# Performance work log

Measured on AMD Instinct MI355X. Metric: run time of the kernel, lower is better.

## Reference

```python
import jax, jax.numpy as jnp
import numpy as np

SIZE = 7
SIGMA = 1.5
CHANNELS = 1
K1 = 0.01
K2 = 0.03
NP_ = SIZE * SIZE
COV_NORM = NP_ / (NP_ - 1)


def gaussian_window(size=SIZE, sigma=SIGMA, channels=CHANNELS):
    x = jnp.arange(size, dtype=jnp.float32) - size // 2
    g = jnp.exp(-x ** 2 / (2.0 * sigma ** 2))[None, :]  # [1, size]
    w = (g.T @ g)  # [size, size]
    w = w / jnp.sum(w)
    return jnp.broadcast_to(w[None, None], (channels, 1, size, size))  # [C,1,k,k]


def _blur(x, w, pad):
    # depthwise conv2d, groups == channels
    return jax.lax.conv_general_dilated(
        x, w, window_strides=(1, 1), padding=[(pad, pad), (pad, pad)],
        dimension_numbers=('NCHW', 'OIHW', 'NCHW'),
        feature_group_count=x.shape[1])


def setup_inputs() -> dict:
    key = jax.random.key(0)
    k1, k2 = jax.random.split(key)
    B, C, H, W = 64, CHANNELS, 512, 512
    X = jax.random.uniform(k1, (B, C, H, W), dtype=jnp.float32)
    Y = jax.random.uniform(k2, (B, C, H, W), dtype=jnp.float32)
    window = gaussian_window()
    return {"X": X, "Y": Y, "window": window}


def reference(X, Y, window):
    B = Y.shape[0]
    Yf = Y.reshape(B, -1)
    data_range = (jnp.max(Yf, axis=1) - jnp.min(Yf, axis=1)).reshape(B, 1, 1, 1)
    C1 = (K1 * data_range) ** 2
    C2 = (K2 * data_range) ** 2
    pad = SIZE // 2
    mux = _blur(X, window, pad)
    muy = _blur(Y, window, pad)
    mux_sq = mux * mux
    muy_sq = muy * muy
    muxy = mux * muy
    sigmax_sq = (_blur(X * X, window, pad) - mux_sq) * COV_NORM
    sigmay_sq = (_blur(Y * Y, window, pad) - muy_sq) * COV_NORM
    sigmaxy = (_blur(X * Y, window, pad) - muxy) * COV_NORM
    ssim_map = (2 * muxy + C1) * (2 * sigmaxy + C2) / ((mux_sq + muy_sq + C1) * (sigmax_sq + sigmay_sq + C2))
    return 1.0 - jnp.mean(ssim_map)
```

## Files before the change

### kernel.cpp

```cpp
#include <hip/hip_runtime.h>
#include <math.h>


__device__ __forceinline__ unsigned fkey(float f) {
    unsigned u = __float_as_uint(f);
    return (u & 0x80000000u) ? ~u : (u | 0x80000000u);
}
__device__ __forceinline__ float funkey(unsigned k) {
    return __uint_as_float((k & 0x80000000u) ? (k & 0x7FFFFFFFu) : ~k);
}

__global__ void init_ws(const float* __restrict__ w, float* __restrict__ u7,
                        unsigned* __restrict__ mink, unsigned* __restrict__ maxk,
                        double* __restrict__ sum) {
    int t = threadIdx.x;
    if (t == 0) *sum = 0.0;
    if (t < 64) { mink[t] = 0xFFFFFFFFu; maxk[t] = 0u; }
    if (t < 7) {
        float s = 0.f;
        for (int j = 0; j < 7; ++j) s += w[t * 7 + j];
        u7[t] = s;
    }
}

__global__ __launch_bounds__(256) void minmax_kernel(const float4* __restrict__ Y,
                                                     unsigned* __restrict__ mink,
                                                     unsigned* __restrict__ maxk) {
    int b = blockIdx.x >> 4, ch = blockIdx.x & 15;
    const float4* p = Y + (size_t)b * 65536 + (size_t)ch * 4096 + threadIdx.x;
    float lmin = INFINITY, lmax = -INFINITY;
#pragma unroll
    for (int i = 0; i < 16; ++i) {
        float4 v = p[(size_t)i * 256];
        lmin = fminf(lmin, fminf(fminf(v.x, v.y), fminf(v.z, v.w)));
        lmax = fmaxf(lmax, fmaxf(fmaxf(v.x, v.y), fmaxf(v.z, v.w)));
    }
#pragma unroll
    for (int off = 32; off; off >>= 1) {
        lmin = fminf(lmin, __shfl_down(lmin, off));
        lmax = fmaxf(lmax, __shfl_down(lmax, off));
    }
    if ((threadIdx.x & 63) == 0) {
        atomicMin(&mink[b], fkey(lmin));
        atomicMax(&maxk[b], fkey(lmax));
    }
}

__global__ __launch_bounds__(256, 4) void ssim_kernel(const float* __restrict__ X,
                                                      const float* __restrict__ Yg,
                                                      const float* __restrict__ u7,
                                                      const unsigned* __restrict__ mink,
                                                      const unsigned* __restrict__ maxk,
                                                      double* __restrict__ sum) {
    __shared__ float2 s[2][264];
    __shared__ float warpsum[4];

    const int blk = blockIdx.x;
    const int b   = blk >> 5;
    const int sub = blk & 31;
    const int cs  = sub & 1;
    const int rs  = sub >> 1;
    const int c0  = cs << 8;
    const int r0  = rs << 5;
    const int t   = threadIdx.x;

    float u[7];
#pragma unroll
    for (int i = 0; i < 7; ++i) u[i] = u7[i];

    const float dr = funkey(maxk[b]) - funkey(mink[b]);
    float C1 = 0.01f * dr; C1 *= C1;
    float C2 = 0.03f * dr; C2 *= C2;
    const float cn = 49.f / 48.f;

    const float* __restrict__ Xb = X  + ((size_t)b << 18);
    const float* __restrict__ Yb = Yg + ((size_t)b << 18);

    const int  c    = c0 + t;
    const bool hasE = (t < 6);
    const int  eL   = (t < 3) ? t : (t + 256);
    const int  ecol = c0 + eL - 3;
    const bool eok  = (ecol >= 0) && (ecol < 512);
    const int  ec   = min(max(ecol, 0), 511);

    float pxr[2], pyr[2], pxe[2], pye[2];
    float phx[7], phy[7], phxx[7], phyy[7], phxy[7];
    float ssacc = 0.f;

#define LOADROW(P, JJ) do {                                                   \
    int r_ = r0 - 3 + (JJ);                                                   \
    if (r_ >= 0 && r_ < 512) {                                                \
        const float* xp_ = Xb + ((size_t)r_ << 9);                            \
        const float* yp_ = Yb + ((size_t)r_ << 9);                            \
        pxr[(P)] = xp_[c]; pyr[(P)] = yp_[c];                                 \
        if (hasE) { pxe[(P)] = eok ? xp_[ec] : 0.f;                           \
                    pye[(P)] = eok ? yp_[ec] : 0.f; }                         \
    } else {                                                                  \
        pxr[(P)] = 0.f; pyr[(P)] = 0.f; pxe[(P)] = 0.f; pye[(P)] = 0.f;       \
    }                                                                         \
} while (0)

#define WRITEROW(P) do {                                                      \
    s[(P)][t + 3] = make_float2(pxr[(P)], pyr[(P)]);                          \
    if (hasE) s[(P)][eL] = make_float2(pxe[(P)], pye[(P)]);                   \
} while (0)

#define HBLUR(BUF, SLOT) do {                                                 \
    float hx_ = 0.f, hy_ = 0.f, hxx_ = 0.f, hyy_ = 0.f, hxy_ = 0.f;           \
    _Pragma("unroll")                                                         \
    for (int k_ = 0; k_ < 7; ++k_) {                                          \
        float2 v_ = s[(BUF)][t + k_];                                         \
        float wx_ = u[k_] * v_.x, wy_ = u[k_] * v_.y;                         \
        hx_ += wx_; hy_ += wy_;                                               \
        hxx_ = fmaf(wx_, v_.x, hxx_);                                         \
        hxy_ = fmaf(wx_, v_.y, hxy_);                                         \
        hyy_ = fmaf(wy_, v_.y, hyy_);                                         \
    }                                                                         \
    phx[(SLOT)] = hx_; phy[(SLOT)] = hy_;                                     \
    phxx[(SLOT)] = hxx_; phyy[(SLOT)] = hyy_; phxy[(SLOT)] = hxy_;            \
} while (0)

#define VS(a, J) fmaf(u[6], a[(J) % 7], fmaf(u[5], a[((J)+6) % 7],            \
               fmaf(u[4], a[((J)+5) % 7], fmaf(u[3], a[((J)+4) % 7],          \
               fmaf(u[2], a[((J)+3) % 7], fmaf(u[1], a[((J)+2) % 7],          \
               u[0] * a[((J)+1) % 7]))))))

#define EMIT(J) do {                                                          \
    float mux = VS(phx, (J)), muy = VS(phy, (J));                             \
    float mxx = VS(phxx, (J)), myy = VS(phyy, (J)), mxy = VS(phxy, (J));      \
    float mux2 = mux * mux, muy2 = muy * muy, muxy = mux * muy;               \
    float sxx = (mxx - mux2) * cn;                                            \
    float syy = (myy - muy2) * cn;                                            \
    float sxy = (mxy - muxy) * cn;                                            \
    float num = (2.f * muxy + C1) * (2.f * sxy + C2);                         \
    float den = (mux2 + muy2 + C1) * (sxx + syy + C2);                        \
    ssacc = fmaf(num, __builtin_amdgcn_rcpf(den), ssacc);                     \
} while (0)

#define PSTEP(J) do {                                                         \
    HBLUR((J) & 1, (J) % 7);                                                  \
    WRITEROW(((J) + 1) & 1);                                                  \
    LOADROW(((J) + 1) & 1, (J) + 3);                                          \
    __syncthreads();                                                          \
} while (0)

#define MSTEP(J) do {                                                         \
    HBLUR((J) & 1, (J) % 7);                                                  \
    EMIT(J);                                                                  \
    WRITEROW(((J) + 1) & 1);                                                  \
    LOADROW(((J) + 1) & 1, jb + (J) + 3);                                     \
    __syncthreads();                                                          \
} while (0)

#define MSTEP_NL(J) do {                                  \
    HBLUR((J) & 1, (J) % 7);                                                  \
    EMIT(J);                                                                  \
    WRITEROW(((J) + 1) & 1);                                                  \
    __syncthreads();                                                          \
} while (0)

#define MSTEP_END(J) do {                 \
    HBLUR((J) & 1, (J) % 7);                                                  \
    EMIT(J);                                                                  \
} while (0)

    LOADROW(0, 0);
    LOADROW(1, 1);
    WRITEROW(0);
    LOADROW(0, 2);
    __syncthreads();

    PSTEP(0); PSTEP(1); PSTEP(2); PSTEP(3); PSTEP(4); PSTEP(5);

    for (int g = 0; g < 2; ++g) {
        const int jb = 14 * g;
        MSTEP(6);  MSTEP(7);  MSTEP(8);  MSTEP(9);  MSTEP(10); MSTEP(11); MSTEP(12);
        MSTEP(13); MSTEP(14); MSTEP(15); MSTEP(16); MSTEP(17); MSTEP(18); MSTEP(19);
    }

    {
        const int jb = 28;
        MSTEP(6);
        MSTEP_NL(7);
        MSTEP_NL(8);
        MSTEP_END(9);
    }

#undef LOADROW
#undef WRITEROW
#undef HBLUR
#undef VS
#undef EMIT
#undef PSTEP
#undef MSTEP
#undef MSTEP_NL
#undef MSTEP_END

#pragma unroll
    for (int off = 32; off; off >>= 1) ssacc += __shfl_down(ssacc, off);
    if ((t & 63) == 0) warpsum[t >> 6] = ssacc;
    __syncthreads();
    if (t == 0) {
        double sm = (double)warpsum[0] + (double)warpsum[1] +
                    (double)warpsum[2] + (double)warpsum[3];
        atomicAdd(sum, sm);
    }
}

__global__ void finalize_kernel(const double* __restrict__ sum, float* __restrict__ out) {
    out[0] = (float)(1.0 - (*sum) / (64.0 * 512.0 * 512.0));
}

extern "C" void kernel_launch(void* const* d_in, const int* in_sizes, int n_in,
                              void* d_out, int out_size, void* d_ws, size_t ws_size,
                              hipStream_t stream) {
    const float* X = (const float*)d_in[0];
    const float* Y = (const float*)d_in[1];
    const float* W = (const float*)d_in[2];

    char* ws = (char*)d_ws;
    double* sum = (double*)(ws + 0);
    unsigned* mink = (unsigned*)(ws + 16);
    unsigned* maxk = (unsigned*)(ws + 16 + 256);
    float* u7 = (float*)(ws + 16 + 512);

    init_ws<<<1, 64, 0, stream>>>(W, u7, mink, maxk, sum);
    minmax_kernel<<<1024, 256, 0, stream>>>((const float4*)Y, mink, maxk);
    ssim_kernel<<<2048, 256, 0, stream>>>(X, Y, u7, mink, maxk, sum);
    finalize_kernel<<<1, 1, 0, stream>>>(sum, (float*)d_out);
}
```

Measured before the change: 93.63 us.

## Process two columns per thread with full-row blocks and float2 loads

Each thread now computes two adjacent output columns and each block covers the full 512-column row, so the column-halo exchange and the edge-thread loads go away. Global loads become float2 and shared-memory rows are stored as float4 with zero padding, which lets eight loaded values feed two horizontal blurs. The grid is halved and the occupancy hint is removed from the launch bounds. In exchange, each thread holds twice as many partial sums in registers, which may lower occupancy.

```diff
diff --git a/kernel.cpp b/kernel.cpp
--- a/kernel.cpp
+++ b/kernel.cpp
@@ -46,21 +46,18 @@
     }
 }
 
-__global__ __launch_bounds__(256, 4) void ssim_kernel(const float* __restrict__ X,
-                                                      const float* __restrict__ Yg,
-                                                      const float* __restrict__ u7,
-                                                      const unsigned* __restrict__ mink,
-                                                      const unsigned* __restrict__ maxk,
-                                                      double* __restrict__ sum) {
-    __shared__ float2 s[2][264];
+__global__ __launch_bounds__(256) void ssim_kernel(const float* __restrict__ X,
+                                                   const float* __restrict__ Yg,
+                                                   const float* __restrict__ u7,
+                                                   const unsigned* __restrict__ mink,
+                                                   const unsigned* __restrict__ maxk,
+                                                   double* __restrict__ sum) {
+    __shared__ float4 s4[2][260];
     __shared__ float warpsum[4];
 
     const int blk = blockIdx.x;
-    const int b   = blk >> 5;
-    const int sub = blk & 31;
-    const int cs  = sub & 1;
-    const int rs  = sub >> 1;
-    const int c0  = cs << 8;
+    const int b   = blk >> 4;
+    const int rs  = blk & 15;
     const int r0  = rs << 5;
     const int t   = threadIdx.x;
 
@@ -76,48 +73,62 @@
     const float* __restrict__ Xb = X  + ((size_t)b << 18);
     const float* __restrict__ Yb = Yg + ((size_t)b << 18);
 
-    const int  c    = c0 + t;
-    const bool hasE = (t < 6);
-    const int  eL   = (t < 3) ? t : (t + 256);
-    const int  ecol = c0 + eL - 3;
-    const bool eok  = (ecol >= 0) && (ecol < 512);
-    const int  ec   = min(max(ecol, 0), 511);
-
-    float pxr[2], pyr[2], pxe[2], pye[2];
-    float phx[7], phy[7], phxx[7], phyy[7], phxy[7];
+    if (t < 2) {
+        float4 z = make_float4(0.f, 0.f, 0.f, 0.f);
+        s4[0][t] = z; s4[1][t] = z;
+        s4[0][258 + t] = z; s4[1][258 + t] = z;
+    }
+
+    float2 fx[2], fy[2];
+    float phx0[7], phy0[7], phxx0[7], phyy0[7], phxy0[7];
+    float phx1[7], phy1[7], phxx1[7], phyy1[7], phxy1[7];
     float ssacc = 0.f;
 
 #define LOADROW(P, JJ) do {                                                   \
     int r_ = r0 - 3 + (JJ);                                                   \
-    if (r_ >= 0 && r_ < 512) {                                                \
-        const float* xp_ = Xb + ((size_t)r_ << 9);                            \
-        const float* yp_ = Yb + ((size_t)r_ << 9);                            \
-        pxr[(P)] = xp_[c]; pyr[(P)] = yp_[c];                                 \
-        if (hasE) { pxe[(P)] = eok ? xp_[ec] : 0.f;                           \
-                    pye[(P)] = eok ? yp_[ec] : 0.f; }                         \
+    if (r_ >= 0 && r_ < 512) {                      \
+        const float2* xp_ = (const float2*)(Xb + ((size_t)r_ << 9)) + t;      \
+        const float2* yp_ = (const float2*)(Yb + ((size_t)r_ << 9)) + t;      \
+        fx[(P)] = *xp_; fy[(P)] = *yp_;                                       \
     } else {                                                                  \
-        pxr[(P)] = 0.f; pyr[(P)] = 0.f; pxe[(P)] = 0.f; pye[(P)] = 0.f;       \
+        fx[(P)] = make_float2(0.f, 0.f); fy[(P)] = make_float2(0.f, 0.f);     \
     }                                                                         \
 } while (0)
 
 #define WRITEROW(P) do {                                                      \
-    s[(P)][t + 3] = make_float2(pxr[(P)], pyr[(P)]);                          \
-    if (hasE) s[(P)][eL] = make_float2(pxe[(P)], pye[(P)]);                   \
+    s4[(P)][t + 2] = make_float4(fx[(P)].x, fy[(P)].x, fx[(P)].y, fy[(P)].y); \
 } while (0)
 
 #define HBLUR(BUF, SLOT) do {                                                 \
-    float hx_ = 0.f, hy_ = 0.f, hxx_ = 0.f, hyy_ = 0.f, hxy_ = 0.f;           \
+    const float2* sb_ = (const float2*)s4[(BUF)];                             \
+    float2 v_[8];                                                             \
     _Pragma("unroll")                                                         \
-    for (int k_ = 0; k_ < 7; ++k_) {                                          \
-        float2 v_ = s[(BUF)][t + k_];                                         \
-        float wx_ = u[k_] * v_.x, wy_ = u[k_] * v_.y;                         \
-        hx_ += wx_; hy_ += wy_;                                               \
-        hxx_ = fmaf(wx_, v_.x, hxx_);                                         \
-        hxy_ = fmaf(wx_, v_.y, hxy_);                                         \
-        hyy_ = fmaf(wy_, v_.y, hyy_);                                         \
-    }                                                                         \
-    phx[(SLOT)] = hx_; phy[(SLOT)] = hy_;                                     \
-    phxx[(SLOT)] = hxx_; phyy[(SLOT)] = hyy_; phxy[(SLOT)] = hxy_;            \
+    for (int k_ = 0; k_ < 8; ++k_) v_[k_] = sb_[(t << 1) + 1 + k_];           \
+    float hx0_=0.f, hy0_=0.f, hxx0_=0.f, hyy0_=0.f, hxy0_=0.f;                \
+    float hx1_=0.f, hy1_=0.f, hxx1_=0.f, hyy1_=0.f, hxy1_=0.f;                \
+    _Pragma("unroll")                                                         \
+    for (int k_ = 0; k_ < 8; ++k_) {                                          \
+        float xv_ = v_[k_].x, yv_ = v_[k_].y;                                 \
+        float xx_ = xv_ * xv_, yy_ = yv_ * yv_, xy_ = xv_ * yv_;              \
+        if (k_ < 7) {                                                         \
+            hx0_  = fmaf(u[k_], xv_, hx0_);                                   \
+            hy0_  = fmaf(u[k_], yv_, hy0_);                                   \
+            hxx0_ = fmaf(u[k_], xx_, hxx0_);                                  \
+            hyy0_ = fmaf(u[k_], yy_, hyy0_);                                  \
+            hxy0_ = fmaf(u[k_], xy_, hxy0_);                                  \
+        }                                                                     \
+        if (k_ > 0) {                                                         \
+            hx1_  = fmaf(u[k_ - 1], xv_, hx1_);                               \
+            hy1_  = fmaf(u[k_ - 1], yv_, hy1_);                               \
+            hxx1_ = fmaf(u[k_ - 1], xx_, hxx1_);                              \
+            hyy1_ = fmaf(u[k_ - 1], yy_, hyy1_);                              \
+            hxy1_ = fmaf(u[k_ - 1], xy_, hxy1_);                              \
+        }                                                                     \
+    }                                                                         \
+    phx0[(SLOT)] = hx0_; phy0[(SLOT)] = hy0_; phxx0[(SLOT)] = hxx0_;          \
+    phyy0[(SLOT)] = hyy0_; phxy0[(SLOT)] = hxy0_;                             \
+    phx1[(SLOT)] = hx1_; phy1[(SLOT)] = hy1_; phxx1[(SLOT)] = hxx1_;          \
+    phyy1[(SLOT)] = hyy1_; phxy1[(SLOT)] = hxy1_;                             \
 } while (0)
 
 #define VS(a, J) fmaf(u[6], a[(J) % 7], fmaf(u[5], a[((J)+6) % 7],            \
@@ -125,16 +136,27 @@
                fmaf(u[2], a[((J)+3) % 7], fmaf(u[1], a[((J)+2) % 7],          \
                u[0] * a[((J)+1) % 7]))))))
 
-#define EMIT(J) do {                                                          \
-    float mux = VS(phx, (J)), muy = VS(phy, (J));                             \
-    float mxx = VS(phxx, (J)), myy = VS(phyy, (J)), mxy = VS(phxy, (J));      \
-    float mux2 = mux * mux, muy2 = muy * muy, muxy = mux * muy;               \
-    float sxx = (mxx - mux2) * cn;                                            \
-    float syy = (myy - muy2) * cn;                                            \
-    float sxy = (mxy - muxy) * cn;                                            \
+#define SSIM1(mux, muy, mxx, myy, mxy) do {                                   \
+    float mux2 = (mux) * (mux), muy2 = (muy) * (muy), muxy = (mux) * (muy);   \
+    float sxx = ((mxx) - mux2) * cn;                                          \
+    float syy = ((myy) - muy2) * cn;                                          \
+    float sxy = ((mxy) - muxy) * cn;                                          \
     float num = (2.f * muxy + C1) * (2.f * sxy + C2);                         \
     float den = (mux2 + muy2 + C1) * (sxx + syy + C2);                        \
     ssacc = fmaf(num, __builtin_amdgcn_rcpf(den), ssacc);                     \
+} while (0)
+
+#define EMIT(J) do {                                                          \
+    {                                                                         \
+        float mux = VS(phx0, (J)), muy = VS(phy0, (J));                       \
+        float mxx = VS(phxx0, (J)), myy = VS(phyy0, (J)), mxy = VS(phxy0, (J));\
+        SSIM1(mux, muy, mxx, myy, mxy);                                       \
+    }                                                                         \
+    {                                                                         \
+        float mux = VS(phx1, (J)), muy = VS(phy1, (J));                       \
+        float mxx = VS(phxx1, (J)), myy = VS(phyy1, (J)), mxy = VS(phxy1, (J));\
+        SSIM1(mux, muy, mxx, myy, mxy);                                       \
+    }                                                                         \
 } while (0)
 
 #define PSTEP(J) do {                                                         \
@@ -152,14 +174,14 @@
     __syncthreads();                                                          \
 } while (0)
 
-#define MSTEP_NL(J) do {                                  \
+#define MSTEP_NL(J) do {                                                      \
     HBLUR((J) & 1, (J) % 7);                                                  \
     EMIT(J);                                                                  \
     WRITEROW(((J) + 1) & 1);                                                  \
     __syncthreads();                                                          \
 } while (0)
 
-#define MSTEP_END(J) do {                 \
+#define MSTEP_END(J) do {                                                     \
     HBLUR((J) & 1, (J) % 7);                                                  \
     EMIT(J);                                                                  \
 } while (0)
@@ -190,6 +212,7 @@
 #undef WRITEROW
 #undef HBLUR
 #undef VS
+#undef SSIM1
 #undef EMIT
 #undef PSTEP
 #undef MSTEP
@@ -226,6 +249,6 @@
 
     init_ws<<<1, 64, 0, stream>>>(W, u7, mink, maxk, sum);
     minmax_kernel<<<1024, 256, 0, stream>>>((const float4*)Y, mink, maxk);
-    ssim_kernel<<<2048, 256, 0, stream>>>(X, Y, u7, mink, maxk, sum);
+    ssim_kernel<<<1024, 256, 0, stream>>>(X, Y, u7, mink, maxk, sum);
     finalize_kernel<<<1, 1, 0, stream>>>(sum, (float*)d_out);
 }
```

Result: slower. 130.6 us (+39.5%).

## Merge xx and yy blur channels and double the row tile per block

Applied to the files above, without the earlier changes.

The SSIM formula only needs the sum of the x² and y² blurs, so the kernel precomputes x²+y² and x·y per pixel when writing to shared memory. The horizontal and vertical blurs then run over four channels instead of five, using float4 LDS reads. Each block also covers 64 rows instead of 32, which halves the grid and cuts the relative cost of the 6-row halo reloads. The trade-off is fewer blocks to spread across CUs, and a small change in rounding from combining the sums first.

```diff
diff --git a/kernel.cpp b/kernel.cpp
--- a/kernel.cpp
+++ b/kernel.cpp
@@ -52,16 +52,16 @@
                                                       const unsigned* __restrict__ mink,
                                                       const unsigned* __restrict__ maxk,
                                                       double* __restrict__ sum) {
-    __shared__ float2 s[2][264];
+    __shared__ float4 s4[2][262];
     __shared__ float warpsum[4];
 
     const int blk = blockIdx.x;
-    const int b   = blk >> 5;
-    const int sub = blk & 31;
+    const int b   = blk >> 4;
+    const int sub = blk & 15;
     const int cs  = sub & 1;
     const int rs  = sub >> 1;
     const int c0  = cs << 8;
-    const int r0  = rs << 5;
+    const int r0  = rs << 6;
     const int t   = threadIdx.x;
 
     float u[7];
@@ -71,7 +71,8 @@
     const float dr = funkey(maxk[b]) - funkey(mink[b]);
     float C1 = 0.01f * dr; C1 *= C1;
     float C2 = 0.03f * dr; C2 *= C2;
-    const float cn = 49.f / 48.f;
+    const float cn  = 49.f / 48.f;
+    const float cn2 = 2.f * cn;
 
     const float* __restrict__ Xb = X  + ((size_t)b << 18);
     const float* __restrict__ Yb = Yg + ((size_t)b << 18);
@@ -83,41 +84,46 @@
     const bool eok  = (ecol >= 0) && (ecol < 512);
     const int  ec   = min(max(ecol, 0), 511);
 
-    float pxr[2], pyr[2], pxe[2], pye[2];
-    float phx[7], phy[7], phxx[7], phyy[7], phxy[7];
+    float fx[2], fy[2], ex[2], ey[2];
+    float phx[7], phy[7], phq[7], phxy[7];
     float ssacc = 0.f;
 
 #define LOADROW(P, JJ) do {                                                   \
     int r_ = r0 - 3 + (JJ);                                                   \
-    if (r_ >= 0 && r_ < 512) {                                                \
+    if (r_ >= 0 && r_ < 512) {                      \
         const float* xp_ = Xb + ((size_t)r_ << 9);                            \
         const float* yp_ = Yb + ((size_t)r_ << 9);                            \
-        pxr[(P)] = xp_[c]; pyr[(P)] = yp_[c];                                 \
-        if (hasE) { pxe[(P)] = eok ? xp_[ec] : 0.f;                           \
-                    pye[(P)] = eok ? yp_[ec] : 0.f; }                         \
+        fx[(P)] = xp_[c]; fy[(P)] = yp_[c];                                   \
+        if (hasE) { ex[(P)] = eok ? xp_[ec] : 0.f;                            \
+                    ey[(P)] = eok ? yp_[ec] : 0.f; }                          \
     } else {                                                                  \
-        pxr[(P)] = 0.f; pyr[(P)] = 0.f; pxe[(P)] = 0.f; pye[(P)] = 0.f;       \
+        fx[(P)] = 0.f; fy[(P)] = 0.f; ex[(P)] = 0.f; ey[(P)] = 0.f;           \
     }                                                                         \
 } while (0)
 
 #define WRITEROW(P) do {                                                      \
-    s[(P)][t + 3] = make_float2(pxr[(P)], pyr[(P)]);                          \
-    if (hasE) s[(P)][eL] = make_float2(pxe[(P)], pye[(P)]);                   \
+    float q_  = fmaf(fx[(P)], fx[(P)], fy[(P)] * fy[(P)]);                    \
+    float xy_ = fx[(P)] * fy[(P)];                                            \
+    s4[(P)][t + 3] = make_float4(fx[(P)], fy[(P)], q_, xy_);                  \
+    if (hasE) {                                                               \
+        float qe_  = fmaf(ex[(P)], ex[(P)], ey[(P)] * ey[(P)]);               \
+        float xye_ = ex[(P)] * ey[(P)];                                       \
+        s4[(P)][eL] = make_float4(ex[(P)], ey[(P)], qe_, xye_);               \
+    }                                                                         \
 } while (0)
 
 #define HBLUR(BUF, SLOT) do {                                                 \
-    float hx_ = 0.f, hy_ = 0.f, hxx_ = 0.f, hyy_ = 0.f, hxy_ = 0.f;           \
+    float hx_ = 0.f, hy_ = 0.f, hq_ = 0.f, hxy_ = 0.f;                        \
     _Pragma("unroll")                                                         \
     for (int k_ = 0; k_ < 7; ++k_) {                                          \
-        float2 v_ = s[(BUF)][t + k_];                                         \
-        float wx_ = u[k_] * v_.x, wy_ = u[k_] * v_.y;                         \
-        hx_ += wx_; hy_ += wy_;                                               \
-        hxx_ = fmaf(wx_, v_.x, hxx_);                                         \
-        hxy_ = fmaf(wx_, v_.y, hxy_);                                         \
-        hyy_ = fmaf(wy_, v_.y, hyy_);                                         \
+        float4 v_ = s4[(BUF)][t + k_];                                        \
+        hx_  = fmaf(u[k_], v_.x, hx_);                                        \
+        hy_  = fmaf(u[k_], v_.y, hy_);                                        \
+        hq_  = fmaf(u[k_], v_.z, hq_);                                        \
+        hxy_ = fmaf(u[k_], v_.w, hxy_);                                       \
     }                                                                         \
     phx[(SLOT)] = hx_; phy[(SLOT)] = hy_;                                     \
-    phxx[(SLOT)] = hxx_; phyy[(SLOT)] = hyy_; phxy[(SLOT)] = hxy_;            \
+    phq[(SLOT)] = hq_; phxy[(SLOT)] = hxy_;                                   \
 } while (0)
 
 #define VS(a, J) fmaf(u[6], a[(J) % 7], fmaf(u[5], a[((J)+6) % 7],            \
@@ -127,14 +133,14 @@
 
 #define EMIT(J) do {                                                          \
     float mux = VS(phx, (J)), muy = VS(phy, (J));                             \
-    float mxx = VS(phxx, (J)), myy = VS(phyy, (J)), mxy = VS(phxy, (J));      \
+    float mq  = VS(phq, (J)), mxy = VS(phxy, (J));                            \
     float mux2 = mux * mux, muy2 = muy * muy, muxy = mux * muy;               \
-    float sxx = (mxx - mux2) * cn;                                            \
-    float syy = (myy - muy2) * cn;                                            \
-    float sxy = (mxy - muxy) * cn;                                            \
-    float num = (2.f * muxy + C1) * (2.f * sxy + C2);                         \
-    float den = (mux2 + muy2 + C1) * (sxx + syy + C2);                        \
-    ssacc = fmaf(num, __builtin_amdgcn_rcpf(den), ssacc);                     \
+    float m2 = mux2 + muy2;                                                   \
+    float A_ = fmaf(muxy, 2.f, C1);                   \
+    float B_ = fmaf(mxy - muxy, cn2, C2);             \
+    float D_ = m2 + C1;                                                       \
+    float E_ = fmaf(mq - m2, cn, C2);                 \
+    ssacc = fmaf(A_ * B_, __builtin_amdgcn_rcpf(D_ * E_), ssacc);             \
 } while (0)
 
 #define PSTEP(J) do {                                                         \
@@ -152,14 +158,14 @@
     __syncthreads();                                                          \
 } while (0)
 
-#define MSTEP_NL(J) do {                                  \
+#define MSTEP_NL(J) do {                                                      \
     HBLUR((J) & 1, (J) % 7);                                                  \
     EMIT(J);                                                                  \
     WRITEROW(((J) + 1) & 1);                                                  \
     __syncthreads();                                                          \
 } while (0)
 
-#define MSTEP_END(J) do {                 \
+#define MSTEP_END(J) do {                                                     \
     HBLUR((J) & 1, (J) % 7);                                                  \
     EMIT(J);                                                                  \
 } while (0)
@@ -172,18 +178,22 @@
 
     PSTEP(0); PSTEP(1); PSTEP(2); PSTEP(3); PSTEP(4); PSTEP(5);
 
-    for (int g = 0; g < 2; ++g) {
+    for (int g = 0; g < 4; ++g) {
         const int jb = 14 * g;
         MSTEP(6);  MSTEP(7);  MSTEP(8);  MSTEP(9);  MSTEP(10); MSTEP(11); MSTEP(12);
         MSTEP(13); MSTEP(14); MSTEP(15); MSTEP(16); MSTEP(17); MSTEP(18); MSTEP(19);
     }
 
     {
-        const int jb = 28;
+        const int jb = 56;
         MSTEP(6);
-        MSTEP_NL(7);
-        MSTEP_NL(8);
-        MSTEP_END(9);
+        MSTEP(7);
+        MSTEP(8);
+        MSTEP(9);
+        MSTEP(10);
+        MSTEP_NL(11);
+        MSTEP_NL(12);
+        MSTEP_END(13);
     }
 
 #undef LOADROW
@@ -226,6 +236,6 @@
 
     init_ws<<<1, 64, 0, stream>>>(W, u7, mink, maxk, sum);
     minmax_kernel<<<1024, 256, 0, stream>>>((const float4*)Y, mink, maxk);
-    ssim_kernel<<<2048, 256, 0, stream>>>(X, Y, u7, mink, maxk, sum);
+    ssim_kernel<<<1024, 256, 0, stream>>>(X, Y, u7, mink, maxk, sum);
     finalize_kernel<<<1, 1, 0, stream>>>(sum, (float*)d_out);
 }
```

Result: slower. 108.2 us (+15.6%).

## Give each wavefront a private LDS strip and drop block-wide barriers

Applied to the files above, without the earlier changes.

Splits the 256-column block tile into four independent 64-column strips, one per wavefront. Each strip has its own double-buffered LDS rows with a 6-column halo. The per-row __syncthreads calls are removed and replaced by compiler memory barriers, relying on lockstep execution inside a 64-lane wavefront. This removes block-wide synchronisation stalls on every row step. In exchange, each wave loads its own halo columns, so redundant global loads and LDS writes increase, and correctness now depends on wavefront-synchronous LDS ordering.

```diff
diff --git a/kernel.cpp b/kernel.cpp
--- a/kernel.cpp
+++ b/kernel.cpp
@@ -52,17 +52,21 @@
                                                       const unsigned* __restrict__ mink,
                                                       const unsigned* __restrict__ maxk,
                                                       double* __restrict__ sum) {
-    __shared__ float2 s[2][264];
+    __shared__ float2 s[4][2][72];
     __shared__ float warpsum[4];
 
-    const int blk = blockIdx.x;
-    const int b   = blk >> 5;
-    const int sub = blk & 31;
-    const int cs  = sub & 1;
-    const int rs  = sub >> 1;
-    const int c0  = cs << 8;
-    const int r0  = rs << 5;
-    const int t   = threadIdx.x;
+    const int blk  = blockIdx.x;
+    const int b    = blk >> 5;
+    const int sub  = blk & 31;
+    const int cs   = sub & 1;
+    const int rs   = sub >> 1;
+    const int t    = threadIdx.x;
+    const int wv   = t >> 6;
+    const int lane = t & 63;
+    const int c0   = (cs << 8) + (wv << 6);
+    const int r0   = rs << 5;
+
+    float2 (* __restrict__ sw)[72] = s[wv];
 
     float u[7];
 #pragma unroll
@@ -76,40 +80,44 @@
     const float* __restrict__ Xb = X  + ((size_t)b << 18);
     const float* __restrict__ Yb = Yg + ((size_t)b << 18);
 
-    const int  c    = c0 + t;
-    const bool hasE = (t < 6);
-    const int  eL   = (t < 3) ? t : (t + 256);
+    const int  c    = c0 + lane;
+    const bool hasE = (lane < 6);
+    const int  eL   = (lane < 3) ? lane : (lane + 64);
     const int  ecol = c0 + eL - 3;
     const bool eok  = (ecol >= 0) && (ecol < 512);
     const int  ec   = min(max(ecol, 0), 511);
 
-    float pxr[2], pyr[2], pxe[2], pye[2];
+    float fx[2], fy[2], ex[2], ey[2];
     float phx[7], phy[7], phxx[7], phyy[7], phxy[7];
     float ssacc = 0.f;
 
+#define CBAR asm volatile("" ::: "memory")
+
 #define LOADROW(P, JJ) do {                                                   \
     int r_ = r0 - 3 + (JJ);                                                   \
-    if (r_ >= 0 && r_ < 512) {                                                \
+    if (r_ >= 0 && r_ < 512) {                      \
         const float* xp_ = Xb + ((size_t)r_ << 9);                            \
         const float* yp_ = Yb + ((size_t)r_ << 9);                            \
-        pxr[(P)] = xp_[c]; pyr[(P)] = yp_[c];                                 \
-        if (hasE) { pxe[(P)] = eok ? xp_[ec] : 0.f;                           \
-                    pye[(P)] = eok ? yp_[ec] : 0.f; }                         \
+        fx[(P)] = xp_[c]; fy[(P)] = yp_[c];                                   \
+        if (hasE) { ex[(P)] = eok ? xp_[ec] : 0.f;                            \
+                    ey[(P)] = eok ? yp_[ec] : 0.f; }                          \
     } else {                                                                  \
-        pxr[(P)] = 0.f; pyr[(P)] = 0.f; pxe[(P)] = 0.f; pye[(P)] = 0.f;       \
+        fx[(P)] = 0.f; fy[(P)] = 0.f; ex[(P)] = 0.f; ey[(P)] = 0.f;           \
     }                                                                         \
 } while (0)
 
 #define WRITEROW(P) do {                                                      \
-    s[(P)][t + 3] = make_float2(pxr[(P)], pyr[(P)]);                          \
-    if (hasE) s[(P)][eL] = make_float2(pxe[(P)], pye[(P)]);                   \
+    CBAR;                                                                     \
+    sw[(P)][lane + 3] = make_float2(fx[(P)], fy[(P)]);                        \
+    if (hasE) sw[(P)][eL] = make_float2(ex[(P)], ey[(P)]);                    \
+    CBAR;                                                                     \
 } while (0)
 
 #define HBLUR(BUF, SLOT) do {                                                 \
     float hx_ = 0.f, hy_ = 0.f, hxx_ = 0.f, hyy_ = 0.f, hxy_ = 0.f;           \
     _Pragma("unroll")                                                         \
     for (int k_ = 0; k_ < 7; ++k_) {                                          \
-        float2 v_ = s[(BUF)][t + k_];                                         \
+        float2 v_ = sw[(BUF)][lane + k_];                                     \
         float wx_ = u[k_] * v_.x, wy_ = u[k_] * v_.y;                         \
         hx_ += wx_; hy_ += wy_;                                               \
         hxx_ = fmaf(wx_, v_.x, hxx_);                                         \
@@ -141,7 +149,6 @@
     HBLUR((J) & 1, (J) % 7);                                                  \
     WRITEROW(((J) + 1) & 1);                                                  \
     LOADROW(((J) + 1) & 1, (J) + 3);                                          \
-    __syncthreads();                                                          \
 } while (0)
 
 #define MSTEP(J) do {                                                         \
@@ -149,17 +156,15 @@
     EMIT(J);                                                                  \
     WRITEROW(((J) + 1) & 1);                                                  \
     LOADROW(((J) + 1) & 1, jb + (J) + 3);                                     \
-    __syncthreads();                                                          \
-} while (0)
-
-#define MSTEP_NL(J) do {                                  \
+} while (0)
+
+#define MSTEP_NL(J) do {                                                      \
     HBLUR((J) & 1, (J) % 7);                                                  \
     EMIT(J);                                                                  \
     WRITEROW(((J) + 1) & 1);                                                  \
-    __syncthreads();                                                          \
-} while (0)
-
-#define MSTEP_END(J) do {                 \
+} while (0)
+
+#define MSTEP_END(J) do {                                                     \
     HBLUR((J) & 1, (J) % 7);                                                  \
     EMIT(J);                                                                  \
 } while (0)
@@ -168,7 +173,6 @@
     LOADROW(1, 1);
     WRITEROW(0);
     LOADROW(0, 2);
-    __syncthreads();
 
     PSTEP(0); PSTEP(1); PSTEP(2); PSTEP(3); PSTEP(4); PSTEP(5);
 
@@ -186,6 +190,7 @@
         MSTEP_END(9);
     }
 
+#undef CBAR
 #undef LOADROW
 #undef WRITEROW
 #undef HBLUR
@@ -198,7 +203,7 @@
 
 #pragma unroll
     for (int off = 32; off; off >>= 1) ssacc += __shfl_down(ssacc, off);
-    if ((t & 63) == 0) warpsum[t >> 6] = ssacc;
+    if (lane == 0) warpsum[wv] = ssacc;
     __syncthreads();
     if (t == 0) {
         double sm = (double)warpsum[0] + (double)warpsum[1] +
```

Measured after the change: 313.1 us. 234% more time.
